# Kernel optimization log

Measured on AMD Instinct MI355X. Metric: run time of the kernel, lower is better.

## Reference

```python
import jax, jax.numpy as jnp
import numpy as np

VOCAB = 100000
EMB = 128
D = 8
K = 128
SUB = EMB // D  # 16
BN_EPS = 1e-3  # keras BatchNormalization default epsilon


def setup_inputs() -> dict:
    key = jax.random.key(0)
    k1, k2, k3 = jax.random.split(key, 3)
    ids = jax.random.randint(k1, (1024, 128), 0, VOCAB, dtype=jnp.int64)
    query_wemb = jax.random.normal(k2, (VOCAB, EMB), dtype=jnp.float32)
    centroids = jax.random.normal(k3, (D, K, SUB), dtype=jnp.float32)
    return {"ids": ids, "query_wemb": query_wemb, "centroids": centroids}


def reference(ids, query_wemb, centroids):
    d, k, sub = centroids.shape
    emb = d * sub
    flat = ids.reshape(-1)                      # [N]
    x = query_wemb[flat].reshape(-1, d, sub)    # [N, d, sub]

    norm_x = jnp.sum(x * x, axis=-1, keepdims=True)          # [N, d, 1]
    norm_c = jnp.sum(centroids * centroids, axis=-1)[None]   # [1, d, k]
    dot = jnp.einsum('nds,dks->ndk', x, centroids)           # [N, d, k]
    response = -norm_x + 2.0 * dot - norm_c                  # [N, d, k]

    # BatchNorm(scale=False, center=False), training=True: batch stats over
    # axes (0,1), per-k channel (keras default axis=-1)
    mean = jnp.mean(response, axis=(0, 1), keepdims=True)
    var = jnp.var(response, axis=(0, 1), keepdims=True)
    resp_bn = (response - mean) * jax.lax.rsqrt(var + BN_EPS)

    codes = jnp.argmax(resp_bn, axis=-1)                     # [N, d]

    # per-subspace centroid gather (non-shared centroids)
    outputs = centroids[jnp.arange(d)[None, :], codes]       # [N, d, sub]

    # straight-through estimator
    out_st = x + jax.lax.stop_gradient(outputs - x)          # [N, d, sub]
    return out_st.reshape(ids.shape + (emb,))
```

## Files before the change

kernel.cpp:

```cpp
#include <hip/hip_runtime.h>


constexpr int NTOK = 131072;
constexpr int ST   = 2320;
constexpr float EPS = 0.001f;


__global__ __launch_bounds__(256) void k1_stats(const int* __restrict__ ids,
                                                const float* __restrict__ wemb,
                                                float* __restrict__ partials,
                                                int tpb)
{
    __shared__ float xs[32][132];
    __shared__ float nrm[32][8];
    const int t = threadIdx.x;
    const int b = blockIdx.x;

    float g[4][4];
#pragma unroll
    for (int i = 0; i < 4; ++i)
#pragma unroll
        for (int j = 0; j < 4; ++j) g[i][j] = 0.f;
    float sx = 0.f, hh = 0.f, s2 = 0.f;

    const int d_g = t >> 4;
    const int r0  = ((t >> 2) & 3) << 2;
    const int c0  = (t & 3) << 2;
    const int u   = t & 127;
    const int d_s = u >> 4;
    const int s_s = u & 15;

    const int nchunks = tpb >> 5;
    for (int ch = 0; ch < nchunks; ++ch) {
        const int n0 = b * tpb + ch * 32;
#pragma unroll
        for (int rep = 0; rep < 4; ++rep) {
            int i = t + rep * 256;
            int n = i >> 5, f = i & 31;
            int id = ids[n0 + n];
            float4 v = *(const float4*)(wemb + (size_t)id * 128 + f * 4);
            *(float4*)(&xs[n][f * 4]) = v;
        }
        __syncthreads();
        {
            int n = t >> 3, dd = t & 7;
            const float* xp = &xs[n][dd * 16];
            float4 a = *(const float4*)(xp);
            float4 bq = *(const float4*)(xp + 4);
            float4 c = *(const float4*)(xp + 8);
            float4 dq = *(const float4*)(xp + 12);
            float acc = a.x*a.x + a.y*a.y + a.z*a.z + a.w*a.w;
            acc += bq.x*bq.x + bq.y*bq.y + bq.z*bq.z + bq.w*bq.w;
            acc += c.x*c.x + c.y*c.y + c.z*c.z + c.w*c.w;
            acc += dq.x*dq.x + dq.y*dq.y + dq.z*dq.z + dq.w*dq.w;
            nrm[n][dd] = acc;
        }
        __syncthreads();
        if (t < 128) {
            for (int n = 0; n < 32; ++n) {
                const float* xp = &xs[n][d_g * 16];
                float4 av = *(const float4*)(xp + r0);
                float4 bv = *(const float4*)(xp + c0);
                float aa[4] = {av.x, av.y, av.z, av.w};
                float bb[4] = {bv.x, bv.y, bv.z, bv.w};
#pragma unroll
                for (int i = 0; i < 4; ++i)
#pragma unroll
                    for (int j = 0; j < 4; ++j)
                        g[i][j] = fmaf(aa[i], bb[j], g[i][j]);
            }
        } else {
            for (int n = 0; n < 32; ++n) {
                float xv = xs[n][d_s * 16 + s_s];
                float nv = nrm[n][d_s];
                sx += xv;
                hh = fmaf(nv, xv, hh);
                if (s_s == 0) s2 = fmaf(nv, nv, s2);
            }
        }
        __syncthreads();
    }
    float* pb = partials + (size_t)b * ST;
    if (t < 128) {
        const int base = d_g * 256;
#pragma unroll
        for (int i = 0; i < 4; ++i)
#pragma unroll
            for (int j = 0; j < 4; ++j)
                pb[base + (r0 + i) * 16 + (c0 + j)] = g[i][j];
    } else {
        pb[2048 + d_s * 16 + s_s] = sx;
        pb[2176 + d_s * 16 + s_s] = hh;
        if (s_s == 0) pb[2304 + d_s] = s2;
    }
}

__global__ __launch_bounds__(256) void k2a_reduce(float* __restrict__ partials, int nb)
{
    const int idx = blockIdx.x * 256 + threadIdx.x;
    if (idx >= 2312) return;
    const int y = blockIdx.y;
    float acc[8] = {0.f, 0.f, 0.f, 0.f, 0.f, 0.f, 0.f, 0.f};
    int b = y;
    while (b + 7 * 32 < nb) {
#pragma unroll
        for (int u = 0; u < 8; ++u)
            acc[u] += partials[(size_t)(b + u * 32) * ST + idx];
        b += 8 * 32;
    }
    while (b < nb) { acc[0] += partials[(size_t)b * ST + idx]; b += 32; }
    float s = ((acc[0] + acc[1]) + (acc[2] + acc[3]))
            + ((acc[4] + acc[5]) + (acc[6] + acc[7]));
    partials[(size_t)y * ST + idx] = s;
}

__global__ __launch_bounds__(256) void k2b_reduce(const float* __restrict__ partials,
                                                  float* __restrict__ stats)
{
    const int idx = blockIdx.x * 256 + threadIdx.x;
    if (idx >= 2312) return;
    float acc[8] = {0.f, 0.f, 0.f, 0.f, 0.f, 0.f, 0.f, 0.f};
#pragma unroll
    for (int j = 0; j < 4; ++j)
#pragma unroll
        for (int u = 0; u < 8; ++u)
            acc[u] += partials[(size_t)(j * 8 + u) * ST + idx];
    stats[idx] = ((acc[0] + acc[1]) + (acc[2] + acc[3]))
               + ((acc[4] + acc[5]) + (acc[6] + acc[7]));
}

__global__ __launch_bounds__(128) void k3_final(const float* __restrict__ stats,
                                                const float* __restrict__ centroids,
                                                float2* __restrict__ ab)
{
    __shared__ float st[2312];
    const int t = threadIdx.x;
    for (int i = t; i < 2312; i += 128) st[i] = stats[i];
    __syncthreads();
    const int k = t;

    double Sn[8], Sn_tot = 0.0, S2_tot = 0.0;
#pragma unroll
    for (int d = 0; d < 8; ++d) {
        double s = 0.0;
        for (int ss = 0; ss < 16; ++ss) s += (double)st[d * 256 + ss * 17];
        Sn[d] = s; Sn_tot += s;
        S2_tot += (double)st[2304 + d];
    }
    double sr = -Sn_tot, sr2 = S2_tot;
    double ncd[8];
    for (int d = 0; d < 8; ++d) {
        const float* cp = centroids + d * 2048 + k * 16;
        float cv[16];
#pragma unroll
        for (int s = 0; s < 16; ++s) cv[s] = cp[s];
        double nc = 0, cdSx = 0, ch = 0, cGc = 0;
        for (int s = 0; s < 16; ++s) {
            nc   += (double)cv[s] * cv[s];
            cdSx += (double)cv[s] * st[2048 + d * 16 + s];
            ch   += (double)cv[s] * st[2176 + d * 16 + s];
            double rd = 0;
            for (int s2i = 0; s2i < 16; ++s2i)
                rd += (double)st[d * 256 + s * 16 + s2i] * cv[s2i];
            cGc += (double)cv[s] * rd;
        }
        ncd[d] = nc;
        sr  += 2.0 * cdSx - (double)NTOK * nc;
        sr2 += 4.0 * cGc + (double)NTOK * nc * nc + 2.0 * nc * Sn[d]
               - 4.0 * ch - 4.0 * nc * cdSx;
    }
    const double M = (double)NTOK * 8.0;
    double mean = sr / M;
    double var  = sr2 / M - mean * mean;
    float alpha = (float)(1.0 / sqrt(var + (double)EPS));
#pragma unroll
    for (int d = 0; d < 8; ++d) {
        float beta = (float)((double)alpha * (-ncd[d] - mean));
        ab[d * 128 + k] = make_float2(2.f * alpha, beta);
    }
}

__global__ __launch_bounds__(256, 8) void k4_main(const int* __restrict__ ids,
                                                  const float* __restrict__ wemb,
                                                  const float* __restrict__ centroids,
                                                  const float2* __restrict__ ab,
                                                  float* __restrict__ out)
{
    const int t = threadIdx.x;
    const int d = blockIdx.y;
    const int n = blockIdx.x * 256 + t;
    const float* cd = centroids + d * 2048;
    const float2* gb = ab + (size_t)d * 128;

    const float* xp = wemb + (size_t)ids[n] * 128 + d * 16;
    float x[16];
    {
        float4 v0 = *(const float4*)(xp);
        float4 v1 = *(const float4*)(xp + 4);
        float4 v2 = *(const float4*)(xp + 8);
        float4 v3 = *(const float4*)(xp + 12);
        x[0] = v0.x; x[1] = v0.y; x[2]  = v0.z; x[3]  = v0.w;
        x[4] = v1.x; x[5] = v1.y; x[6]  = v1.z; x[7]  = v1.w;
        x[8] = v2.x; x[9] = v2.y; x[10] = v2.z; x[11] = v2.w;
        x[12] = v3.x; x[13] = v3.y; x[14] = v3.z; x[15] = v3.w;
    }
    float s = 0.f;
#pragma unroll
    for (int q = 0; q < 16; ++q) s = fmaf(x[q], x[q], s);
    const float nx2 = -0.5f * s;
    float best = -3.4e38f;
    int code = 0;

#pragma unroll 4
    for (int k = 0; k < 128; ++k) {
        const float* cp = cd + k * 16;
        float acc = nx2;
#pragma unroll
        for (int q = 0; q < 16; ++q) acc = fmaf(cp[q], x[q], acc);
        float2 g = gb[k];
        float score = fmaf(g.x, acc, g.y);
        bool p = score > best;
        best = p ? score : best;
        code = p ? k : code;
    }

    const float* cw = cd + code * 16;
    float* op = out + (size_t)n * 128 + d * 16;
#pragma unroll
    for (int q = 0; q < 16; q += 4) {
        float4 cv = *(const float4*)(cw + q);
        float4 o;
        o.x = x[q + 0] + (cv.x - x[q + 0]);
        o.y = x[q + 1] + (cv.y - x[q + 1]);
        o.z = x[q + 2] + (cv.z - x[q + 2]);
        o.w = x[q + 3] + (cv.w - x[q + 3]);
        *(float4*)(op + q) = o;
    }
}

extern "C" void kernel_launch(void* const* d_in, const int* in_sizes, int n_in,
                              void* d_out, int out_size, void* d_ws, size_t ws_size,
                              hipStream_t stream)
{
    const int* ids    = (const int*)d_in[0];
    const float* wemb = (const float*)d_in[1];
    const float* cent = (const float*)d_in[2];
    float* out = (float*)d_out;
    float* ws  = (float*)d_ws;

    int p1b = 1024;
    if (ws_size < ((size_t)1024 * ST + 2320 + 2048) * 4) p1b = 512;
    if (ws_size < ((size_t)512  * ST + 2320 + 2048) * 4) p1b = 256;
    if (ws_size < ((size_t)256  * ST + 2320 + 2048) * 4) p1b = 128;
    const int tpb = NTOK / p1b;

    float* partials = ws;
    float* stats    = ws + (size_t)p1b * ST;
    float2* ab      = (float2*)(stats + 2320);

    hipLaunchKernelGGL(k1_stats,   dim3(p1b),     dim3(256), 0, stream, ids, wemb, partials, tpb);
    hipLaunchKernelGGL(k2a_reduce, dim3(10, 32),  dim3(256), 0, stream, partials, p1b);
    hipLaunchKernelGGL(k2b_reduce, dim3(10),      dim3(256), 0, stream, partials, stats);
    hipLaunchKernelGGL(k3_final,   dim3(1),       dim3(128), 0, stream, stats, cent, ab);
    hipLaunchKernelGGL(k4_main,    dim3(512, 8),  dim3(256), 0, stream, ids, wemb, cent, ab, out);
}
```

Before: 140.1 us.

## Stage centroids in LDS and process eight tokens per thread in k4

The main kernel now copies the subspace's 128x16 centroids and the BN scale/shift pairs into shared memory once per block. Each thread then handles eight tokens, so every centroid load from LDS is reused across eight dot products. The grid shrinks to 128x8 blocks of 128 threads. In exchange, register pressure rises (128 floats of x per thread), which may lower occupancy and latency hiding for the gathered embedding loads.

```diff
diff --git a/kernel.cpp b/kernel.cpp
--- a/kernel.cpp
+++ b/kernel.cpp
@@ -180,61 +180,95 @@
     }
 }
 
-__global__ __launch_bounds__(256, 8) void k4_main(const int* __restrict__ ids,
-                                                  const float* __restrict__ wemb,
-                                                  const float* __restrict__ centroids,
-                                                  const float2* __restrict__ ab,
-                                                  float* __restrict__ out)
-{
+__global__ __launch_bounds__(128) void k4_main(const int* __restrict__ ids,
+                                               const float* __restrict__ wemb,
+                                               const float* __restrict__ centroids,
+                                               const float2* __restrict__ ab,
+                                               float* __restrict__ out)
+{
+    __shared__ float  cs[128 * 16];
+    __shared__ float2 gbs[128];
+
     const int t = threadIdx.x;
     const int d = blockIdx.y;
-    const int n = blockIdx.x * 256 + t;
-    const float* cd = centroids + d * 2048;
-    const float2* gb = ab + (size_t)d * 128;
-
-    const float* xp = wemb + (size_t)ids[n] * 128 + d * 16;
-    float x[16];
-    {
-        float4 v0 = *(const float4*)(xp);
-        float4 v1 = *(const float4*)(xp + 4);
-        float4 v2 = *(const float4*)(xp + 8);
-        float4 v3 = *(const float4*)(xp + 12);
-        x[0] = v0.x; x[1] = v0.y; x[2]  = v0.z; x[3]  = v0.w;
-        x[4] = v1.x; x[5] = v1.y; x[6]  = v1.z; x[7]  = v1.w;
-        x[8] = v2.x; x[9] = v2.y; x[10] = v2.z; x[11] = v2.w;
-        x[12] = v3.x; x[13] = v3.y; x[14] = v3.z; x[15] = v3.w;
-    }
-    float s = 0.f;
-#pragma unroll
-    for (int q = 0; q < 16; ++q) s = fmaf(x[q], x[q], s);
-    const float nx2 = -0.5f * s;
-    float best = -3.4e38f;
-    int code = 0;
-
-#pragma unroll 4
+    const float* cd = centroids + (size_t)d * 2048;
+
+#pragma unroll
+    for (int i = 0; i < 4; ++i)
+        ((float4*)cs)[t + i * 128] = ((const float4*)cd)[t + i * 128];
+    gbs[t] = ab[(size_t)d * 128 + t];
+
+    const int nbase = blockIdx.x * 1024 + t;
+    float x[8][16];
+    float nx[8], best[8];
+    int   code[8];
+#pragma unroll
+    for (int j = 0; j < 8; ++j) {
+        const int n = nbase + j * 128;
+        const float* xp = wemb + (size_t)ids[n] * 128 + d * 16;
+#pragma unroll
+        for (int q = 0; q < 16; q += 4) {
+            float4 v = *(const float4*)(xp + q);
+            x[j][q] = v.x; x[j][q + 1] = v.y; x[j][q + 2] = v.z; x[j][q + 3] = v.w;
+        }
+        float s = 0.f;
+#pragma unroll
+        for (int q = 0; q < 16; ++q) s = fmaf(x[j][q], x[j][q], s);
+        nx[j] = -0.5f * s;
+        best[j] = -3.4e38f;
+        code[j] = 0;
+    }
+
+    __syncthreads();
+
+#pragma unroll 2
     for (int k = 0; k < 128; ++k) {
-        const float* cp = cd + k * 16;
-        float acc = nx2;
-#pragma unroll
-        for (int q = 0; q < 16; ++q) acc = fmaf(cp[q], x[q], acc);
-        float2 g = gb[k];
-        float score = fmaf(g.x, acc, g.y);
-        bool p = score > best;
-        best = p ? score : best;
-        code = p ? k : code;
-    }
-
-    const float* cw = cd + code * 16;
-    float* op = out + (size_t)n * 128 + d * 16;
-#pragma unroll
-    for (int q = 0; q < 16; q += 4) {
-        float4 cv = *(const float4*)(cw + q);
-        float4 o;
-        o.x = x[q + 0] + (cv.x - x[q + 0]);
-        o.y = x[q + 1] + (cv.y - x[q + 1]);
-        o.z = x[q + 2] + (cv.z - x[q + 2]);
-        o.w = x[q + 3] + (cv.w - x[q + 3]);
-        *(float4*)(op + q) = o;
+        const float4 c0 = *(const float4*)(&cs[k * 16 + 0]);
+        const float4 c1 = *(const float4*)(&cs[k * 16 + 4]);
+        const float4 c2 = *(const float4*)(&cs[k * 16 + 8]);
+        const float4 c3 = *(const float4*)(&cs[k * 16 + 12]);
+        const float2 g  = gbs[k];
+#pragma unroll
+        for (int j = 0; j < 8; ++j) {
+            float acc = nx[j];
+            acc = fmaf(c0.x, x[j][0],  acc);
+            acc = fmaf(c0.y, x[j][1],  acc);
+            acc = fmaf(c0.z, x[j][2],  acc);
+            acc = fmaf(c0.w, x[j][3],  acc);
+            acc = fmaf(c1.x, x[j][4],  acc);
+            acc = fmaf(c1.y, x[j][5],  acc);
+            acc = fmaf(c1.z, x[j][6],  acc);
+            acc = fmaf(c1.w, x[j][7],  acc);
+            acc = fmaf(c2.x, x[j][8],  acc);
+            acc = fmaf(c2.y, x[j][9],  acc);
+            acc = fmaf(c2.z, x[j][10], acc);
+            acc = fmaf(c2.w, x[j][11], acc);
+            acc = fmaf(c3.x, x[j][12], acc);
+            acc = fmaf(c3.y, x[j][13], acc);
+            acc = fmaf(c3.z, x[j][14], acc);
+            acc = fmaf(c3.w, x[j][15], acc);
+            float sc = fmaf(g.x, acc, g.y);
+            bool p = sc > best[j];
+            best[j] = p ? sc : best[j];
+            code[j] = p ? k : code[j];
+        }
+    }
+
+#pragma unroll
+    for (int j = 0; j < 8; ++j) {
+        const int n = nbase + j * 128;
+        const float* cw = cd + code[j] * 16;
+        float* op = out + (size_t)n * 128 + d * 16;
+#pragma unroll
+        for (int q = 0; q < 16; q += 4) {
+            float4 cv = *(const float4*)(cw + q);
+            float4 o;
+            o.x = x[j][q + 0] + (cv.x - x[j][q + 0]);
+            o.y = x[j][q + 1] + (cv.y - x[j][q + 1]);
+            o.z = x[j][q + 2] + (cv.z - x[j][q + 2]);
+            o.w = x[j][q + 3] + (cv.w - x[j][q + 3]);
+            *(float4*)(op + q) = o;
+        }
     }
 }
 
@@ -262,5 +296,5 @@
     hipLaunchKernelGGL(k2a_reduce, dim3(10, 32),  dim3(256), 0, stream, partials, p1b);
     hipLaunchKernelGGL(k2b_reduce, dim3(10),      dim3(256), 0, stream, partials, stats);
     hipLaunchKernelGGL(k3_final,   dim3(1),       dim3(128), 0, stream, stats, cent, ab);
-    hipLaunchKernelGGL(k4_main,    dim3(512, 8),  dim3(256), 0, stream, ids, wemb, cent, ab, out);
-}
+    hipLaunchKernelGGL(k4_main,    dim3(128, 8),  dim3(128), 0, stream, ids, wemb, cent, ab, out);
+}
```

Measured after the change: 148.9 us. +6.3%, slower.
